# Kernel tuning notes

Hardware: AMD Instinct MI355X
Metric: run time of the kernel (lower is better)

## Reference

```python
import jax, jax.numpy as jnp
import numpy as np

P = 256  # patch_size (init kwarg)


def _unfold3s2(g):
    # g: [B,1,P,P] -> [B,9,L], kernel 3, stride 2, torch Unfold ordering (kh outer, kw inner)
    B = g.shape[0]
    n = (P - 3) // 2 + 1
    cols = [g[:, 0, di:di + 2 * n - 1:2, dj:dj + 2 * n - 1:2]
            for di in range(3) for dj in range(3)]  # each [B,n,n]
    return jnp.stack(cols, axis=1).reshape(B, 9, n * n)


def _fold3s2(patches):
    # patches: [..., 9, L] -> [..., P, P], overlap-add (torch Fold, kernel 3, stride 2)
    lead = patches.shape[:-2]
    n = (P - 3) // 2 + 1
    p = patches.reshape(*lead, 3, 3, n, n)
    out = jnp.zeros((*lead, P, P), patches.dtype)
    for di in range(3):
        for dj in range(3):
            out = out.at[..., di:di + 2 * n - 1:2, dj:dj + 2 * n - 1:2].add(p[..., di, dj, :, :])
    return out


def _maxpool3x3(x):
    # MaxPool2d(3, stride=1, padding=1) on NCHW
    return jax.lax.reduce_window(x, -jnp.inf, jax.lax.max,
                                 (1, 1, 3, 3), (1, 1, 1, 1),
                                 [(0, 0), (0, 0), (1, 1), (1, 1)])


def setup_inputs() -> dict:
    key = jax.random.key(0)
    k1, k2 = jax.random.split(key)
    x = jax.random.uniform(k1, (2, 3, P, P), dtype=jnp.float32)
    ref = jax.random.uniform(k2, (2, 3, P, P), dtype=jnp.float32)
    return {"x": x, "ref": ref, "k": 4}


def reference(x, ref, k):
    B = x.shape[0]
    L = ((P - 3) // 2 + 1) ** 2
    # grayscale proxies
    x_gray = jnp.max(_maxpool3x3(x), axis=1, keepdims=True) - jnp.min(x, axis=1, keepdims=True)
    ref_gray = jnp.mean(ref, axis=1, keepdims=True)
    input_patch = _unfold3s2(x_gray)   # [B,9,L]
    ref_patch = _unfold3s2(ref_gray)   # [B,9,L]
    # faithful to original: mean over patch index (dim 2), norm of UNCENTERED patches over dim 1
    input_norm = (input_patch - jnp.mean(input_patch, axis=2, keepdims=True)) \
        / jnp.linalg.norm(input_patch, axis=1, keepdims=True)
    ref_norm = (ref_patch - jnp.mean(ref_patch, axis=2, keepdims=True)) \
        / jnp.linalg.norm(ref_patch, axis=1, keepdims=True)
    ncc = jnp.einsum('bpl,bpm->blm', input_norm, ref_norm)  # [B,L,L]
    _, idx = jax.lax.top_k(ncc, k)                           # idx: [B,L,k]
    # gather best-matching ref patches for all k at once: [B,k,9,L]
    idx_t = jnp.transpose(idx, (0, 2, 1))                    # [B,k,L]
    ind = jnp.broadcast_to(idx_t[:, :, None, :], (B, k, 9, L))
    src = jnp.broadcast_to(ref_patch[:, None], (B, k, 9, L))
    gathered = jnp.take_along_axis(src, ind, axis=3)         # [B,k,9,L]
    folded = _fold3s2(gathered)                              # [B,k,P,P]
    return jnp.concatenate([x, folded], axis=1)              # [B,3+k,P,P]
```

## Files before the change

kernel.cpp:

```cpp
#include <hip/hip_runtime.h>
#include <math.h>
#include <float.h>

#define PSZ 256
#define NPATCH 127
#define L 16129
#define KTOP 4
#define TMAIN 256
#define RPT 2
#define ROWS_PER_BLOCK (TMAIN * RPT)
#define NROWBLK 32
#define NS 32
#define SEGLEN 512
#define MSTRIDE 512
#define ROWPAD 16384
#define GRP 16

static constexpr size_t OFF_REFG = 0;
static constexpr size_t OFF_XG   = OFF_REFG + 2 * PSZ * PSZ;
static constexpr size_t OFF_MUI  = OFF_XG   + 2 * PSZ * PSZ;
static constexpr size_t OFF_MUR  = OFF_MUI  + 20;
static constexpr size_t OFF_A    = OFF_MUR  + 20;
static constexpr size_t OFF_B    = OFF_A    + 290324;
static constexpr size_t OFF_BT   = OFF_B    + 290324;
static constexpr size_t OFF_IDX  = OFF_BT   + 290324;
static constexpr size_t OFF_PV   = OFF_IDX  + 2 * L * 4;
static constexpr size_t OFF_PI   = OFF_PV   + (size_t)2 * NS * ROWPAD * 4;

__device__ __forceinline__ void insg(float rm, int gb,
    float& g0, float& g1, float& g2, float& g3,
    int& i0, int& i1, int& i2, int& i3) {
  bool c0 = rm > g0, c1 = rm > g1, c2 = rm > g2, c3 = rm > g3;
  g3 = c2 ? g2 : (c3 ? rm : g3);  i3 = c2 ? i2 : (c3 ? gb : i3);
  g2 = c1 ? g1 : (c2 ? rm : g2);  i2 = c1 ? i1 : (c2 ? gb : i2);
  g1 = c0 ? g0 : (c1 ? rm : g1);  i1 = c0 ? i0 : (c1 ? gb : i1);
  g0 = c0 ? rm : g0;              i0 = c0 ? gb : i0;
}

__device__ __forceinline__ void ins4c(float v, int m,
    float& v0, float& v1, float& v2, float& v3,
    int& x0, int& x1, int& x2, int& x3) {
  bool c0 = (v > v0) || (v == v0 && m < x0);
  bool c1 = (v > v1) || (v == v1 && m < x1);
  bool c2 = (v > v2) || (v == v2 && m < x2);
  bool c3 = (v > v3) || (v == v3 && m < x3);
  v3 = c2 ? v2 : (c3 ? v : v3);  x3 = c2 ? x2 : (c3 ? m : x3);
  v2 = c1 ? v1 : (c2 ? v : v2);  x2 = c1 ? x1 : (c2 ? m : x2);
  v1 = c0 ? v0 : (c1 ? v : v1);  x1 = c0 ? x0 : (c1 ? m : x1);
  v0 = c0 ? v : v0;              x0 = c0 ? m : x0;
}

__global__ void k12_gray(const float* __restrict__ x, const float* __restrict__ ref,
                         float* __restrict__ ws, float* __restrict__ out) {
  __shared__ float sm[34][35];
  int tile = blockIdx.x & 63;
  int b = blockIdx.x >> 6;
  int ty0 = (tile >> 3) << 5, tx0 = (tile & 7) << 5;
  const float* xb = x + (size_t)b * 3 * 65536;
  const float* rb = ref + (size_t)b * 3 * 65536;
  for (int hid = threadIdx.x; hid < 34 * 34; hid += 256) {
    int hy = hid / 34, hx = hid % 34;
    int gy = ty0 + hy - 1, gx = tx0 + hx - 1;
    float m = -FLT_MAX;
    if (gy >= 0 && gy < 256 && gx >= 0 && gx < 256) {
      int pix = gy * 256 + gx;
      m = fmaxf(fmaxf(xb[pix], xb[65536 + pix]), xb[131072 + pix]);
    }
    sm[hy][hx] = m;
  }
  __syncthreads();
  for (int iid = threadIdx.x; iid < 1024; iid += 256) {
    int iy = iid >> 5, ix = iid & 31;
    int gy = ty0 + iy, gx = tx0 + ix;
    int pix = gy * 256 + gx;
    float c0 = xb[pix], c1 = xb[65536 + pix], c2 = xb[131072 + pix];
    float cmin = fminf(fminf(c0, c1), c2);
    float mx = sm[iy][ix];
#pragma unroll
    for (int dy = 0; dy < 3; ++dy)
#pragma unroll
      for (int dx = 0; dx < 3; ++dx)
        mx = fmaxf(mx, sm[iy + dy][ix + dx]);
    size_t id = ((size_t)b << 16) + pix;
    ws[OFF_XG + id] = mx - cmin;
    ws[OFF_REFG + id] = (rb[pix] + rb[65536 + pix] + rb[131072 + pix]) / 3.0f;
    float* ob = out + (size_t)b * 7 * 65536 + pix;
    ob[0] = c0; ob[65536] = c1; ob[131072] = c2;
  }
}

__global__ void k4_mean(float* __restrict__ ws) {
  __shared__ double sm[1024];
  int which = blockIdx.x / 18;
  int bp = blockIdx.x % 18;
  int b = bp / 9, p = bp % 9;
  int di = p / 3, dj = p % 3;
  const float* g = ws + (which ? OFF_REFG : OFF_XG) + ((size_t)b << 16);
  int t = threadIdx.x;
  double s = 0.0;
  int l0 = t * 16;
  if (l0 < L) {
    int l1 = l0 + 16 < L ? l0 + 16 : L;
    int i = l0 / NPATCH, j = l0 % NPATCH;
    for (int l = l0; l < l1; ++l) {
      s += (double)g[(2 * i + di) * PSZ + 2 * j + dj];
      if (++j == NPATCH) { j = 0; ++i; }
    }
  }
  sm[t] = s;
  __syncthreads();
  for (int st = 512; st > 0; st >>= 1) {
    if (t < st) sm[t] += sm[t + st];
    __syncthreads();
  }
  if (t == 0)
    ws[(which ? OFF_MUR : OFF_MUI) + bp] = (float)(sm[0] / (double)L);
}

__global__ void k5_norm(float* __restrict__ ws) {
  int id = blockIdx.x * 256 + threadIdx.x;
  if (id >= 2 * L) return;
  int b = id / L, l = id % L;
  int i = l / NPATCH, j = l % NPATCH;
  const float* xg = ws + OFF_XG + ((size_t)b << 16);
  const float* rg = ws + OFF_REFG + ((size_t)b << 16);
  float vi[9], vr[9];
  float si = 0.f, sr = 0.f;
#pragma unroll
  for (int p = 0; p < 9; ++p) {
    int di = p / 3, dj = p % 3;
    vi[p] = xg[(2 * i + di) * PSZ + 2 * j + dj];
    vr[p] = rg[(2 * i + di) * PSZ + 2 * j + dj];
    si += vi[p] * vi[p];
    sr += vr[p] * vr[p];
  }
  float ni = sqrtf(si), nr = sqrtf(sr);
#pragma unroll
  for (int p = 0; p < 9; ++p) {
    float mi = ws[OFF_MUI + b * 9 + p];
    float mr = ws[OFF_MUR + b * 9 + p];
    float bn = (vr[p] - mr) / nr;
    ws[OFF_A + ((size_t)b * L + l) * 9 + p] = (vi[p] - mi) / ni;
    ws[OFF_B + ((size_t)b * 9 + p) * L + l] = bn;
    ws[OFF_BT + ((size_t)b * L + l) * 9 + p] = bn;
  }
}

__global__ __launch_bounds__(TMAIN, 2) void k6_topk(float* __restrict__ ws) {
  __shared__ float lds[9 * MSTRIDE];

  int bid = blockIdx.x;
  int seg = bid & (NS - 1);
  int rowblk = (bid >> 5) & (NROWBLK - 1);
  int b = bid >> 10;
  int m0 = seg << 9;
  int mend = m0 + SEGLEN;
  if (mend > L) mend = L;
  int mlen = mend - m0;

  const float* Bg = ws + OFF_B + (size_t)b * 9 * L + m0;
  for (int p = 0; p < 9; ++p)
    for (int mm = threadIdx.x; mm < mlen; mm += TMAIN)
      lds[p * MSTRIDE + mm] = Bg[(size_t)p * L + mm];
  __syncthreads();

  int row0 = rowblk * ROWS_PER_BLOCK + threadIdx.x * RPT;
  int r0 = row0 < L - 1 ? row0 : L - 1;
  int r1 = row0 + 1 < L - 1 ? row0 + 1 : L - 1;
  float a0[9], a1[9];
  {
    const float* Ap0 = ws + OFF_A + ((size_t)b * L + r0) * 9;
    const float* Ap1 = ws + OFF_A + ((size_t)b * L + r1) * 9;
#pragma unroll
    for (int p = 0; p < 9; ++p) { a0[p] = Ap0[p]; a1[p] = Ap1[p]; }
  }

  float g00 = -FLT_MAX, g01 = g00, g02 = g00, g03 = g00;
  float g10 = g00, g11 = g00, g12 = g00, g13 = g00;
  int i00 = 0, i01 = 0, i02 = 0, i03 = 0;
  int i10 = 0, i11 = 0, i12 = 0, i13 = 0;

  int nfull = mlen >> 4;
  for (int g = 0; g < nfull; ++g) {
    int mm = g << 4;
    float rm0 = -FLT_MAX, rm1 = -FLT_MAX;
#pragma unroll
    for (int q = 0; q < 4; ++q) {
      float s00, s01, s02, s03, s10, s11, s12, s13;
#pragma unroll
      for (int p = 0; p < 9; ++p) {
        const float4 bq = *reinterpret_cast<const float4*>(&lds[p * MSTRIDE + mm + q * 4]);
        if (p == 0) {
          s00 = a0[0] * bq.x; s01 = a0[0] * bq.y; s02 = a0[0] * bq.z; s03 = a0[0] * bq.w;
          s10 = a1[0] * bq.x; s11 = a1[0] * bq.y; s12 = a1[0] * bq.z; s13 = a1[0] * bq.w;
        } else {
          s00 = fmaf(a0[p], bq.x, s00); s01 = fmaf(a0[p], bq.y, s01);
          s02 = fmaf(a0[p], bq.z, s02); s03 = fmaf(a0[p], bq.w, s03);
          s10 = fmaf(a1[p], bq.x, s10); s11 = fmaf(a1[p], bq.y, s11);
          s12 = fmaf(a1[p], bq.z, s12); s13 = fmaf(a1[p], bq.w, s13);
        }
      }
      rm0 = fmaxf(rm0, fmaxf(fmaxf(s00, s01), fmaxf(s02, s03)));
      rm1 = fmaxf(rm1, fmaxf(fmaxf(s10, s11), fmaxf(s12, s13)));
    }
    int gb = m0 + mm;
    insg(rm0, gb, g00, g01, g02, g03, i00, i01, i02, i03);
    insg(rm1, gb, g10, g11, g12, g13, i10, i11, i12, i13);
  }
  int tb = nfull << 4;
  if (tb < mlen) {
    float rt0 = -FLT_MAX, rt1 = -FLT_MAX;
    for (int mm = tb; mm < mlen; ++mm) {
      float bb = lds[mm];
      float sv0 = a0[0] * bb, sv1 = a1[0] * bb;
#pragma unroll
      for (int p = 1; p < 9; ++p) {
        bb = lds[p * MSTRIDE + mm];
        sv0 = fmaf(a0[p], bb, sv0); sv1 = fmaf(a1[p], bb, sv1);
      }
      rt0 = fmaxf(rt0, sv0); rt1 = fmaxf(rt1, sv1);
    }
    insg(rt0, m0 + tb, g00, g01, g02, g03, i00, i01, i02, i03);
    insg(rt1, m0 + tb, g10, g11, g12, g13, i10, i11, i12, i13);
  }

  int* wsi = (int*)ws;
  if (row0 < L) {
    size_t base = (((size_t)b * NS + seg) * ROWPAD + row0) * 4;
    ws[OFF_PV + base + 0] = g00; ws[OFF_PV + base + 1] = g01;
    ws[OFF_PV + base + 2] = g02; ws[OFF_PV + base + 3] = g03;
    wsi[OFF_PI + base + 0] = i00; wsi[OFF_PI + base + 1] = i01;
    wsi[OFF_PI + base + 2] = i02; wsi[OFF_PI + base + 3] = i03;
  }
  if (row0 + 1 < L) {
    size_t base = (((size_t)b * NS + seg) * ROWPAD + row0 + 1) * 4;
    ws[OFF_PV + base + 0] = g10; ws[OFF_PV + base + 1] = g11;
    ws[OFF_PV + base + 2] = g12; ws[OFF_PV + base + 3] = g13;
    wsi[OFF_PI + base + 0] = i10; wsi[OFF_PI + base + 1] = i11;
    wsi[OFF_PI + base + 2] = i12; wsi[OFF_PI + base + 3] = i13;
  }
}

__global__ void k7_merge(float* __restrict__ ws) {
  int id = blockIdx.x * 256 + threadIdx.x;
  if (id >= 2 * L) return;
  int b = id / L, row = id % L;
  const int* wsi_c = (const int*)ws;

  float v0 = -FLT_MAX, v1 = v0, v2 = v0, v3 = v0;
  int x0 = 0x7FFFFFFF, x1 = x0, x2 = x0, x3 = x0;
  for (int s = 0; s < NS; ++s) {
    size_t base = (((size_t)b * NS + s) * ROWPAD + row) * 4;
#pragma unroll
    for (int q = 0; q < 4; ++q) {
      float val = ws[OFF_PV + base + q];
      int gb = wsi_c[OFF_PI + base + q];
      ins4c(val, gb, v0, v1, v2, v3, x0, x1, x2, x3);
    }
  }

  float a[9];
  const float* Ap = ws + OFF_A + ((size_t)b * L + row) * 9;
#pragma unroll
  for (int p = 0; p < 9; ++p) a[p] = Ap[p];

  int gbs[4] = {x0, x1, x2, x3};
  float w0 = -FLT_MAX, w1 = w0, w2 = w0, w3 = w0;
  int y0 = 0x7FFFFFFF, y1 = y0, y2 = y0, y3 = y0;
#pragma unroll
  for (int slot = 0; slot < 4; ++slot) {
    int gb = gbs[slot];
    int se = ((gb >> 9) + 1) << 9;
    int ge = gb + GRP;
    if (ge > se) ge = se;
    if (ge > L) ge = L;
    for (int mm = gb; mm < ge; ++mm) {
      const float* bt = ws + OFF_BT + ((size_t)b * L + mm) * 9;
      float s = a[0] * bt[0];
#pragma unroll
      for (int p = 1; p < 9; ++p) s = fmaf(a[p], bt[p], s);
      ins4c(s, mm, w0, w1, w2, w3, y0, y1, y2, y3);
    }
  }
  int* wsi = (int*)ws;
  size_t ib = OFF_IDX + (size_t)id * 4;
  wsi[ib] = y0; wsi[ib + 1] = y1; wsi[ib + 2] = y2; wsi[ib + 3] = y3;
}

__global__ void k8_fold(const float* __restrict__ ws, float* __restrict__ out) {
  int id = blockIdx.x * 256 + threadIdx.x;
  if (id >= 2 * KTOP * PSZ * PSZ) return;
  int b = id / (KTOP * PSZ * PSZ);
  int rem = id % (KTOP * PSZ * PSZ);
  int kk = rem >> 16;
  int pix = rem & 0xFFFF;
  int y = pix >> 8, xx = pix & 255;
  const int* wsi = (const int*)ws;
  const float* rg = ws + OFF_REFG + ((size_t)b << 16);
  float acc = 0.f;
  for (int di = 0; di < 3; ++di) {
    int yy = y - di;
    if (yy < 0 || (yy & 1) || (yy >> 1) >= NPATCH) continue;
    int i = yy >> 1;
    for (int dj = 0; dj < 3; ++dj) {
      int xc = xx - dj;
      if (xc < 0 || (xc & 1) || (xc >> 1) >= NPATCH) continue;
      int j = xc >> 1;
      int l = i * NPATCH + j;
      int m = wsi[OFF_IDX + ((size_t)b * L + l) * 4 + kk];
      int mi = m / NPATCH, mj = m % NPATCH;
      acc += rg[(2 * mi + di) * PSZ + 2 * mj + dj];
    }
  }
  out[(((size_t)b * 7 + 3 + kk) * PSZ + y) * PSZ + xx] = acc;
}

extern "C" void kernel_launch(void* const* d_in, const int* in_sizes, int n_in,
                              void* d_out, int out_size, void* d_ws, size_t ws_size,
                              hipStream_t stream) {
  const float* x = (const float*)d_in[0];
  const float* ref = (const float*)d_in[1];
  float* ws = (float*)d_ws;
  float* out = (float*)d_out;

  k12_gray<<<128, 256, 0, stream>>>(x, ref, ws, out);
  k4_mean<<<36, 1024, 0, stream>>>(ws);
  k5_norm<<<(2 * L + 255) / 256, 256, 0, stream>>>(ws);
  k6_topk<<<2 * NROWBLK * NS, TMAIN, 0, stream>>>(ws);
  k7_merge<<<(2 * L + 255) / 256, 256, 0, stream>>>(ws);
  k8_fold<<<(2 * KTOP * PSZ * PSZ + 255) / 256, 256, 0, stream>>>(ws, out);
}
```

Before: 226.8 us.

## Vectorize gray, pad patch rows to 12 floats, fold all k per thread

The gray kernel now has each thread handle 4 adjacent pixels with float4 loads and stores, and it shares the column maxima of the 3x3 max pool across them. The A and BT patch arrays are padded to 12 floats per row so k5_norm can write them, and k6_topk and k7_merge can read them, as aligned float4 vectors. The fold kernel now computes all 4 top-k outputs per pixel from a single int4 index load, which cuts thread count and index reads. The costs are extra workspace and a larger per-row stride. Most time is probably spent in the topk kernel, which changes only in its small A load.

```diff
diff --git a/kernel.cpp b/kernel.cpp
--- a/kernel.cpp
+++ b/kernel.cpp
@@ -15,15 +15,16 @@
 #define MSTRIDE 512
 #define ROWPAD 16384
 #define GRP 16
+#define APAD 12
 
 static constexpr size_t OFF_REFG = 0;
 static constexpr size_t OFF_XG   = OFF_REFG + 2 * PSZ * PSZ;
 static constexpr size_t OFF_MUI  = OFF_XG   + 2 * PSZ * PSZ;
 static constexpr size_t OFF_MUR  = OFF_MUI  + 20;
 static constexpr size_t OFF_A    = OFF_MUR  + 20;
-static constexpr size_t OFF_B    = OFF_A    + 290324;
+static constexpr size_t OFF_B    = OFF_A    + (size_t)2 * L * APAD;
 static constexpr size_t OFF_BT   = OFF_B    + 290324;
-static constexpr size_t OFF_IDX  = OFF_BT   + 290324;
+static constexpr size_t OFF_IDX  = OFF_BT   + (size_t)2 * L * APAD;
 static constexpr size_t OFF_PV   = OFF_IDX  + 2 * L * 4;
 static constexpr size_t OFF_PI   = OFF_PV   + (size_t)2 * NS * ROWPAD * 4;
 
@@ -69,24 +70,41 @@
     sm[hy][hx] = m;
   }
   __syncthreads();
-  for (int iid = threadIdx.x; iid < 1024; iid += 256) {
-    int iy = iid >> 5, ix = iid & 31;
-    int gy = ty0 + iy, gx = tx0 + ix;
-    int pix = gy * 256 + gx;
-    float c0 = xb[pix], c1 = xb[65536 + pix], c2 = xb[131072 + pix];
-    float cmin = fminf(fminf(c0, c1), c2);
-    float mx = sm[iy][ix];
-#pragma unroll
-    for (int dy = 0; dy < 3; ++dy)
-#pragma unroll
-      for (int dx = 0; dx < 3; ++dx)
-        mx = fmaxf(mx, sm[iy + dy][ix + dx]);
-    size_t id = ((size_t)b << 16) + pix;
-    ws[OFF_XG + id] = mx - cmin;
-    ws[OFF_REFG + id] = (rb[pix] + rb[65536 + pix] + rb[131072 + pix]) / 3.0f;
-    float* ob = out + (size_t)b * 7 * 65536 + pix;
-    ob[0] = c0; ob[65536] = c1; ob[131072] = c2;
-  }
+  int t4 = threadIdx.x * 4;
+  int iy = t4 >> 5, ix = t4 & 31;
+  int gy = ty0 + iy, gx = tx0 + ix;
+  int pix = gy * 256 + gx;
+  float4 c0 = *(const float4*)(xb + pix);
+  float4 c1 = *(const float4*)(xb + 65536 + pix);
+  float4 c2 = *(const float4*)(xb + 131072 + pix);
+  float4 r0 = *(const float4*)(rb + pix);
+  float4 r1 = *(const float4*)(rb + 65536 + pix);
+  float4 r2 = *(const float4*)(rb + 131072 + pix);
+  float cm[7];
+#pragma unroll
+  for (int c = 0; c < 7; ++c)
+    cm[c] = fmaxf(fmaxf(sm[iy][ix + c], sm[iy + 1][ix + c]), sm[iy + 2][ix + c]);
+  float cc0[4] = {c0.x, c0.y, c0.z, c0.w};
+  float cc1[4] = {c1.x, c1.y, c1.z, c1.w};
+  float cc2[4] = {c2.x, c2.y, c2.z, c2.w};
+  float rr0[4] = {r0.x, r0.y, r0.z, r0.w};
+  float rr1[4] = {r1.x, r1.y, r1.z, r1.w};
+  float rr2[4] = {r2.x, r2.y, r2.z, r2.w};
+  float xgv[4], rgv[4];
+#pragma unroll
+  for (int k = 0; k < 4; ++k) {
+    float cmin = fminf(fminf(cc0[k], cc1[k]), cc2[k]);
+    float mx = fmaxf(fmaxf(cm[k], cm[k + 1]), cm[k + 2]);
+    xgv[k] = mx - cmin;
+    rgv[k] = (rr0[k] + rr1[k] + rr2[k]) / 3.0f;
+  }
+  size_t id0 = ((size_t)b << 16) + pix;
+  *(float4*)(ws + OFF_XG + id0) = make_float4(xgv[0], xgv[1], xgv[2], xgv[3]);
+  *(float4*)(ws + OFF_REFG + id0) = make_float4(rgv[0], rgv[1], rgv[2], rgv[3]);
+  float* ob = out + (size_t)b * 7 * 65536 + pix;
+  *(float4*)(ob) = c0;
+  *(float4*)(ob + 65536) = c1;
+  *(float4*)(ob + 131072) = c2;
 }
 
 __global__ void k4_mean(float* __restrict__ ws) {
@@ -135,15 +153,26 @@
     sr += vr[p] * vr[p];
   }
   float ni = sqrtf(si), nr = sqrtf(sr);
+  float an[12], btn[12];
 #pragma unroll
   for (int p = 0; p < 9; ++p) {
     float mi = ws[OFF_MUI + b * 9 + p];
     float mr = ws[OFF_MUR + b * 9 + p];
     float bn = (vr[p] - mr) / nr;
-    ws[OFF_A + ((size_t)b * L + l) * 9 + p] = (vi[p] - mi) / ni;
+    an[p] = (vi[p] - mi) / ni;
+    btn[p] = bn;
     ws[OFF_B + ((size_t)b * 9 + p) * L + l] = bn;
-    ws[OFF_BT + ((size_t)b * L + l) * 9 + p] = bn;
-  }
+  }
+  an[9] = an[10] = an[11] = 0.f;
+  btn[9] = btn[10] = btn[11] = 0.f;
+  float4* Ap4 = (float4*)(ws + OFF_A + (size_t)(b * L + l) * APAD);
+  Ap4[0] = make_float4(an[0], an[1], an[2], an[3]);
+  Ap4[1] = make_float4(an[4], an[5], an[6], an[7]);
+  Ap4[2] = make_float4(an[8], an[9], an[10], an[11]);
+  float4* Bt4 = (float4*)(ws + OFF_BT + (size_t)(b * L + l) * APAD);
+  Bt4[0] = make_float4(btn[0], btn[1], btn[2], btn[3]);
+  Bt4[1] = make_float4(btn[4], btn[5], btn[6], btn[7]);
+  Bt4[2] = make_float4(btn[8], btn[9], btn[10], btn[11]);
 }
 
 __global__ __launch_bounds__(TMAIN, 2) void k6_topk(float* __restrict__ ws) {
@@ -169,10 +198,14 @@
   int r1 = row0 + 1 < L - 1 ? row0 + 1 : L - 1;
   float a0[9], a1[9];
   {
-    const float* Ap0 = ws + OFF_A + ((size_t)b * L + r0) * 9;
-    const float* Ap1 = ws + OFF_A + ((size_t)b * L + r1) * 9;
-#pragma unroll
-    for (int p = 0; p < 9; ++p) { a0[p] = Ap0[p]; a1[p] = Ap1[p]; }
+    const float4* Ap0 = (const float4*)(ws + OFF_A + ((size_t)b * L + r0) * APAD);
+    const float4* Ap1 = (const float4*)(ws + OFF_A + ((size_t)b * L + r1) * APAD);
+    float4 u0 = Ap0[0], u1 = Ap0[1], u2 = Ap0[2];
+    float4 w0 = Ap1[0], w1 = Ap1[1], w2 = Ap1[2];
+    a0[0] = u0.x; a0[1] = u0.y; a0[2] = u0.z; a0[3] = u0.w;
+    a0[4] = u1.x; a0[5] = u1.y; a0[6] = u1.z; a0[7] = u1.w; a0[8] = u2.x;
+    a1[0] = w0.x; a1[1] = w0.y; a1[2] = w0.z; a1[3] = w0.w;
+    a1[4] = w1.x; a1[5] = w1.y; a1[6] = w1.z; a1[7] = w1.w; a1[8] = w2.x;
   }
 
   float g00 = -FLT_MAX, g01 = g00, g02 = g00, g03 = g00;
@@ -260,9 +293,12 @@
   }
 
   float a[9];
-  const float* Ap = ws + OFF_A + ((size_t)b * L + row) * 9;
-#pragma unroll
-  for (int p = 0; p < 9; ++p) a[p] = Ap[p];
+  {
+    const float4* Ap4 = (const float4*)(ws + OFF_A + ((size_t)b * L + row) * APAD);
+    float4 u0 = Ap4[0], u1 = Ap4[1], u2 = Ap4[2];
+    a[0] = u0.x; a[1] = u0.y; a[2] = u0.z; a[3] = u0.w;
+    a[4] = u1.x; a[5] = u1.y; a[6] = u1.z; a[7] = u1.w; a[8] = u2.x;
+  }
 
   int gbs[4] = {x0, x1, x2, x3};
   float w0 = -FLT_MAX, w1 = w0, w2 = w0, w3 = w0;
@@ -275,10 +311,12 @@
     if (ge > se) ge = se;
     if (ge > L) ge = L;
     for (int mm = gb; mm < ge; ++mm) {
-      const float* bt = ws + OFF_BT + ((size_t)b * L + mm) * 9;
-      float s = a[0] * bt[0];
-#pragma unroll
-      for (int p = 1; p < 9; ++p) s = fmaf(a[p], bt[p], s);
+      const float4* bt4 = (const float4*)(ws + OFF_BT + ((size_t)b * L + mm) * APAD);
+      float4 b0 = bt4[0], b1 = bt4[1], b2 = bt4[2];
+      float s = a[0] * b0.x;
+      s = fmaf(a[1], b0.y, s); s = fmaf(a[2], b0.z, s); s = fmaf(a[3], b0.w, s);
+      s = fmaf(a[4], b1.x, s); s = fmaf(a[5], b1.y, s); s = fmaf(a[6], b1.z, s);
+      s = fmaf(a[7], b1.w, s); s = fmaf(a[8], b2.x, s);
       ins4c(s, mm, w0, w1, w2, w3, y0, y1, y2, y3);
     }
   }
@@ -289,15 +327,13 @@
 
 __global__ void k8_fold(const float* __restrict__ ws, float* __restrict__ out) {
   int id = blockIdx.x * 256 + threadIdx.x;
-  if (id >= 2 * KTOP * PSZ * PSZ) return;
-  int b = id / (KTOP * PSZ * PSZ);
-  int rem = id % (KTOP * PSZ * PSZ);
-  int kk = rem >> 16;
-  int pix = rem & 0xFFFF;
+  if (id >= 2 * PSZ * PSZ) return;
+  int b = id >> 16;
+  int pix = id & 0xFFFF;
   int y = pix >> 8, xx = pix & 255;
   const int* wsi = (const int*)ws;
   const float* rg = ws + OFF_REFG + ((size_t)b << 16);
-  float acc = 0.f;
+  float acc0 = 0.f, acc1 = 0.f, acc2 = 0.f, acc3 = 0.f;
   for (int di = 0; di < 3; ++di) {
     int yy = y - di;
     if (yy < 0 || (yy & 1) || (yy >> 1) >= NPATCH) continue;
@@ -307,12 +343,18 @@
       if (xc < 0 || (xc & 1) || (xc >> 1) >= NPATCH) continue;
       int j = xc >> 1;
       int l = i * NPATCH + j;
-      int m = wsi[OFF_IDX + ((size_t)b * L + l) * 4 + kk];
-      int mi = m / NPATCH, mj = m % NPATCH;
-      acc += rg[(2 * mi + di) * PSZ + 2 * mj + dj];
-    }
-  }
-  out[(((size_t)b * 7 + 3 + kk) * PSZ + y) * PSZ + xx] = acc;
+      const int4 m4 = *(const int4*)(wsi + OFF_IDX + ((size_t)b * L + l) * 4);
+      acc0 += rg[(2 * (m4.x / NPATCH) + di) * PSZ + 2 * (m4.x % NPATCH) + dj];
+      acc1 += rg[(2 * (m4.y / NPATCH) + di) * PSZ + 2 * (m4.y % NPATCH) + dj];
+      acc2 += rg[(2 * (m4.z / NPATCH) + di) * PSZ + 2 * (m4.z % NPATCH) + dj];
+      acc3 += rg[(2 * (m4.w / NPATCH) + di) * PSZ + 2 * (m4.w % NPATCH) + dj];
+    }
+  }
+  float* ob = out + ((size_t)b * 7 + 3) * 65536 + pix;
+  ob[0] = acc0;
+  ob[65536] = acc1;
+  ob[2 * 65536] = acc2;
+  ob[3 * 65536] = acc3;
 }
 
 extern "C" void kernel_launch(void* const* d_in, const int* in_sizes, int n_in,
@@ -328,5 +370,5 @@
   k5_norm<<<(2 * L + 255) / 256, 256, 0, stream>>>(ws);
   k6_topk<<<2 * NROWBLK * NS, TMAIN, 0, stream>>>(ws);
   k7_merge<<<(2 * L + 255) / 256, 256, 0, stream>>>(ws);
-  k8_fold<<<(2 * KTOP * PSZ * PSZ + 255) / 256, 256, 0, stream>>>(ws, out);
-}
+  k8_fold<<<(2 * PSZ * PSZ + 255) / 256, 256, 0, stream>>>(ws, out);
+}
```

New measurement: 228.3 us. Within noise of the previous version (+0.7%).
